# Kernel optimization log

Measured on AMD Instinct MI355X. Metric: run time of the kernel, lower is better.

## Reference

```python
import jax, jax.numpy as jnp
import numpy as np

L, D, H, EXP = 6, 512, 8, 4
DH = D // H
EPS = 1e-3  # keras LayerNormalization default epsilon


def _layer_norm(x, gamma, beta):
    mu = jnp.mean(x, axis=-1, keepdims=True)
    var = jnp.mean(jnp.square(x - mu), axis=-1, keepdims=True)
    return (x - mu) * jax.lax.rsqrt(var + EPS) * gamma + beta


def setup_inputs() -> dict:
    key = jax.random.key(0)
    ks = jax.random.split(key, 10)
    B, S = 8, 1024
    s_attn = 1.0 / np.sqrt(D)
    s_ffn1 = 1.0 / np.sqrt(D)
    s_ffn2 = 1.0 / np.sqrt(D * EXP)
    return {
        "x": jax.random.normal(ks[0], (B, S, D), dtype=jnp.float32),
        "Wq": jax.random.normal(ks[1], (L, D, D), dtype=jnp.float32) * s_attn,
        "Wk": jax.random.normal(ks[2], (L, D, D), dtype=jnp.float32) * s_attn,
        "Wv": jax.random.normal(ks[3], (L, D, D), dtype=jnp.float32) * s_attn,
        "Wo": jax.random.normal(ks[4], (L, D, D), dtype=jnp.float32) * s_attn,
        "W1": jax.random.normal(ks[5], (L, D, D * EXP), dtype=jnp.float32) * s_ffn1,
        "b1": jnp.zeros((L, D * EXP), dtype=jnp.float32),
        "W2": jax.random.normal(ks[6], (L, D * EXP, D), dtype=jnp.float32) * s_ffn2,
        "b2": jnp.zeros((L, D), dtype=jnp.float32),
        "g_attn": jnp.ones((L, D), dtype=jnp.float32),
        "be_attn": jnp.zeros((L, D), dtype=jnp.float32),
        "g_ffn": jnp.ones((L, D), dtype=jnp.float32),
        "be_ffn": jnp.zeros((L, D), dtype=jnp.float32),
    }


def _self_attention(y, wq, wk, wv, wo):
    B, S, _ = y.shape
    q = (y @ wq).reshape(B, S, H, DH)
    k = (y @ wk).reshape(B, S, H, DH)
    v = (y @ wv).reshape(B, S, H, DH)
    scores = jnp.einsum("bqhd,bkhd->bhqk", q, k) / np.sqrt(float(DH))
    attn = jax.nn.softmax(scores, axis=-1)
    z = jnp.einsum("bhqk,bkhd->bqhd", attn, v).reshape(B, S, D)
    return z @ wo


def reference(x, Wq, Wk, Wv, Wo, W1, b1, W2, b2, g_attn, be_attn, g_ffn, be_ffn):
    encoded = x
    for l in range(L):
        # pre-LN self-attention + residual (dropout=identity at inference)
        attended = _layer_norm(encoded, g_attn[l], be_attn[l])
        attended = _self_attention(attended, Wq[l], Wk[l], Wv[l], Wo[l])
        attended = encoded + attended
        # pre-LN FFN + residual
        h = _layer_norm(attended, g_ffn[l], be_ffn[l])
        h = jax.nn.relu(h @ W1[l] + b1[l]) @ W2[l] + b2[l]
        encoded = attended + h
    return encoded
```

## Files before the change

kernel.cpp:

```cpp
#include <hip/hip_runtime.h>


#define SEQ 1024
#define ROWS 8192
#define QKVW 1536

using bf16x8 = __attribute__((ext_vector_type(8))) short;
using f32x4  = __attribute__((ext_vector_type(4))) float;

__device__ __forceinline__ unsigned short f2bf(float f) {
  union { float f; unsigned u; } v; v.f = f;
  unsigned r = v.u + 0x7FFFu + ((v.u >> 16) & 1u);
  return (unsigned short)(r >> 16);
}

__device__ __forceinline__ float exp2_fast(float x) {
  float r;
  asm("v_exp_f32 %0, %1" : "=v"(r) : "v"(x));
  return r;
}

__device__ __forceinline__ unsigned cvtpk_bf16(float a, float b) {
  unsigned r;
  asm("v_cvt_pk_bf16_f32 %0, %1, %2" : "=v"(r) : "v"(a), "v"(b));
  return r;
}

__device__ __forceinline__ void gl16(const void* g, void* l) {
  typedef const unsigned int __attribute__((address_space(1)))* GP;
  typedef unsigned int __attribute__((address_space(3)))* LP;
  __builtin_amdgcn_global_load_lds((GP)g, (LP)l, 16, 0, 0);
}

__global__ __launch_bounds__(256) void transpose_cast_k(
    const float* __restrict__ W, unsigned short* __restrict__ Wt,
    int K, int N, int lstride, float scale)
{
  __shared__ float tile[32][33];
  const int l = blockIdx.z;
  const float* Wl = W + (size_t)l * K * N;
  unsigned short* Wtl = Wt + (size_t)l * lstride;
  const int k0 = blockIdx.y * 32, n0 = blockIdx.x * 32;
  const int tx = threadIdx.x & 31, ty = threadIdx.x >> 5;
  #pragma unroll
  for (int i = ty; i < 32; i += 8)
    tile[i][tx] = Wl[(size_t)(k0 + i) * N + n0 + tx];
  __syncthreads();
  #pragma unroll
  for (int i = ty; i < 32; i += 8)
    Wtl[(size_t)(n0 + i) * K + k0 + tx] = f2bf(tile[tx][i] * scale);
}

__global__ __launch_bounds__(256) void ln_k(
    const float* __restrict__ x, const float* __restrict__ g,
    const float* __restrict__ be, unsigned short* __restrict__ y, int rows)
{
  const int wid = (blockIdx.x << 2) | (threadIdx.x >> 6);
  const int lane = threadIdx.x & 63;
  if (wid >= rows) return;
  const float4* xr = reinterpret_cast<const float4*>(x + (size_t)wid * 512);
  float4 a = xr[lane];
  float4 b = xr[lane + 64];
  float s = a.x + a.y + a.z + a.w + b.x + b.y + b.z + b.w;
  #pragma unroll
  for (int m = 32; m >= 1; m >>= 1) s += __shfl_xor(s, m);
  const float mu = s * (1.0f / 512.0f);
  const float d0 = a.x - mu, d1 = a.y - mu, d2 = a.z - mu, d3 = a.w - mu;
  const float e0 = b.x - mu, e1 = b.y - mu, e2 = b.z - mu, e3 = b.w - mu;
  float q = d0*d0 + d1*d1 + d2*d2 + d3*d3 + e0*e0 + e1*e1 + e2*e2 + e3*e3;
  #pragma unroll
  for (int m = 32; m >= 1; m >>= 1) q += __shfl_xor(q, m);
  const float inv = rsqrtf(q * (1.0f / 512.0f) + 1e-3f);
  const float4* gr = reinterpret_cast<const float4*>(g);
  const float4* br = reinterpret_cast<const float4*>(be);
  const float4 g0 = gr[lane], g1 = gr[lane + 64];
  const float4 h0 = br[lane], h1 = br[lane + 64];
  ushort4 o0, o1;
  o0.x = f2bf(d0 * inv * g0.x + h0.x);
  o0.y = f2bf(d1 * inv * g0.y + h0.y);
  o0.z = f2bf(d2 * inv * g0.z + h0.z);
  o0.w = f2bf(d3 * inv * g0.w + h0.w);
  o1.x = f2bf(e0 * inv * g1.x + h1.x);
  o1.y = f2bf(e1 * inv * g1.y + h1.y);
  o1.z = f2bf(e2 * inv * g1.z + h1.z);
  o1.w = f2bf(e3 * inv * g1.w + h1.w);
  *reinterpret_cast<ushort4*>(y + (size_t)wid * 512 + lane * 4) = o0;
  *reinterpret_cast<ushort4*>(y + (size_t)wid * 512 + (lane + 64) * 4) = o1;
}

template<bool RELU, bool HASBIAS, bool HASRES, bool OUTBF>
__global__ __launch_bounds__(256) void gemm128_k(
    const unsigned short* __restrict__ A,
    const unsigned short* __restrict__ Wt,
    const float* __restrict__ bias,
    const float* __restrict__ res,
    void* __restrict__ outp, int M, int N, int K)
{
  __shared__ __align__(16) unsigned short As0[4096], Bs0[4096];
  __shared__ __align__(16) unsigned short As1[4096], Bs1[4096];
  const int t = threadIdx.x;
  const int nwg = gridDim.x * gridDim.y;
  const int bid = blockIdx.y * gridDim.x + blockIdx.x;
  const int nid = (bid & 7) * (nwg >> 3) + (bid >> 3);
  const int bx = nid % gridDim.x, by = nid / gridDim.x;
  const int m0 = by * 128, n0 = bx * 128;
  const int w = t >> 6, lane = t & 63, llo = lane & 15, lhi = lane >> 4;
  const int wr = w >> 1, wc = w & 1;

  const int sr = t >> 2, sg = (t & 3) ^ ((t >> 3) & 3);
  const unsigned short* pa = &A[(size_t)(m0 + sr) * K + sg * 8];
  const unsigned short* pb = &Wt[(size_t)(n0 + sr) * K + sg * 8];

#define GSTAGE128(AsX, BsX, koff) do { \
    gl16(pa + (koff), &AsX[t * 8]); \
    gl16(pa + (size_t)64 * K + (koff), &AsX[2048 + t * 8]); \
    gl16(pb + (koff), &BsX[t * 8]); \
    gl16(pb + (size_t)64 * K + (koff), &BsX[2048 + t * 8]); \
  } while (0)

  const int pgo = (lhi ^ ((llo >> 1) & 3)) * 8;

#define GCOMP128(AsX, BsX) do { \
    bf16x8 af[4], bfr[4]; \
    _Pragma("unroll") \
    for (int f = 0; f < 4; f++) { \
      af[f]  = *reinterpret_cast<const bf16x8*>(&AsX[(wr * 64 + f * 16 + llo) * 32 + pgo]); \
      bfr[f] = *reinterpret_cast<const bf16x8*>(&BsX[(wc * 64 + f * 16 + llo) * 32 + pgo]); \
    } \
    _Pragma("unroll") \
    for (int fi = 0; fi < 4; fi++) \
      _Pragma("unroll") \
      for (int fj = 0; fj < 4; fj++) \
        acc[fi][fj] = __builtin_amdgcn_mfma_f32_16x16x32_bf16(af[fi], bfr[fj], acc[fi][fj], 0, 0, 0); \
  } while (0)

  f32x4 acc[4][4] = {};
  GSTAGE128(As0, Bs0, 0);
  for (int k0 = 0; k0 < K; k0 += 64) {
    __syncthreads();
    GSTAGE128(As1, Bs1, k0 + 32);
    GCOMP128(As0, Bs0);
    __syncthreads();
    if (k0 + 64 < K) GSTAGE128(As0, Bs0, k0 + 64);
    GCOMP128(As1, Bs1);
  }
#undef GSTAGE128
#undef GCOMP128

  const int row0 = m0 + wr * 64, col0 = n0 + wc * 64;
  #pragma unroll
  for (int fi = 0; fi < 4; fi++)
    #pragma unroll
    for (int fj = 0; fj < 4; fj++)
      #pragma unroll
      for (int i = 0; i < 4; i++) {
        const int row = row0 + fi * 16 + lhi * 4 + i;
        const int col = col0 + fj * 16 + llo;
        float v = acc[fi][fj][i];
        if (HASBIAS) v += bias[col];
        if (HASRES)  v += res[(size_t)row * N + col];
        if (RELU)    v = fmaxf(v, 0.0f);
        if (OUTBF) ((unsigned short*)outp)[(size_t)row * N + col] = f2bf(v);
        else       ((float*)outp)[(size_t)row * N + col] = v;
      }
}

template<bool RELU, bool HASBIAS, bool HASRES, bool OUTBF>
__global__ __launch_bounds__(256) void gemm64_k(
    const unsigned short* __restrict__ A,
    const unsigned short* __restrict__ Wt,
    const float* __restrict__ bias,
    const float* __restrict__ res,
    void* __restrict__ outp, int M, int N, int K)
{
  __shared__ __align__(16) unsigned short As0[2048], Bs0[4096];
  __shared__ __align__(16) unsigned short As1[2048], Bs1[4096];
  const int t = threadIdx.x;
  const int nwg = gridDim.x * gridDim.y;
  const int bid = blockIdx.y * gridDim.x + blockIdx.x;
  const int nid = (bid & 7) * (nwg >> 3) + (bid >> 3);
  const int bx = nid % gridDim.x, by = nid / gridDim.x;
  const int m0 = by * 64, n0 = bx * 128;
  const int w = t >> 6, lane = t & 63, llo = lane & 15, lhi = lane >> 4;
  const int wr = w >> 1, wc = w & 1;

  const int sr = t >> 2, sg = (t & 3) ^ ((t >> 3) & 3);
  const unsigned short* pa = &A[(size_t)(m0 + sr) * K + sg * 8];
  const unsigned short* pb = &Wt[(size_t)(n0 + sr) * K + sg * 8];

#define GSTAGE64(AsX, BsX, koff) do { \
    gl16(pa + (koff), &AsX[t * 8]); \
    gl16(pb + (koff), &BsX[t * 8]); \
    gl16(pb + (size_t)64 * K + (koff), &BsX[2048 + t * 8]); \
  } while (0)

  const int pgo = (lhi ^ ((llo >> 1) & 3)) * 8;

#define GCOMP64(AsX, BsX) do { \
    bf16x8 af[2], bfr[4]; \
    _Pragma("unroll") \
    for (int f = 0; f < 2; f++) \
      af[f] = *reinterpret_cast<const bf16x8*>(&AsX[(wr * 32 + f * 16 + llo) * 32 + pgo]); \
    _Pragma("unroll") \
    for (int f = 0; f < 4; f++) \
      bfr[f] = *reinterpret_cast<const bf16x8*>(&BsX[(wc * 64 + f * 16 + llo) * 32 + pgo]); \
    _Pragma("unroll") \
    for (int fi = 0; fi < 2; fi++) \
      _Pragma("unroll") \
      for (int fj = 0; fj < 4; fj++) \
        acc[fi][fj] = __builtin_amdgcn_mfma_f32_16x16x32_bf16(af[fi], bfr[fj], acc[fi][fj], 0, 0, 0); \
  } while (0)

  f32x4 acc[2][4] = {};
  GSTAGE64(As0, Bs0, 0);
  for (int k0 = 0; k0 < K; k0 += 64) {
    __syncthreads();
    GSTAGE64(As1, Bs1, k0 + 32);
    GCOMP64(As0, Bs0);
    __syncthreads();
    if (k0 + 64 < K) GSTAGE64(As0, Bs0, k0 + 64);
    GCOMP64(As1, Bs1);
  }
#undef GSTAGE64
#undef GCOMP64

  const int row0 = m0 + wr * 32, col0 = n0 + wc * 64;
  #pragma unroll
  for (int fi = 0; fi < 2; fi++)
    #pragma unroll
    for (int fj = 0; fj < 4; fj++)
      #pragma unroll
      for (int i = 0; i < 4; i++) {
        const int row = row0 + fi * 16 + lhi * 4 + i;
        const int col = col0 + fj * 16 + llo;
        float v = acc[fi][fj][i];
        if (HASBIAS) v += bias[col];
        if (HASRES)  v += res[(size_t)row * N + col];
        if (RELU)    v = fmaxf(v, 0.0f);
        if (OUTBF) ((unsigned short*)outp)[(size_t)row * N + col] = f2bf(v);
        else       ((float*)outp)[(size_t)row * N + col] = v;
      }
}

__global__ __launch_bounds__(256) void vtrans_k(
    const unsigned short* __restrict__ QKV, unsigned short* __restrict__ VT)
{
  __shared__ unsigned short tile[64][66];
  const int kt = blockIdx.x, bh = blockIdx.y;
  const int bb = bh >> 3, h = bh & 7;
  const int t = threadIdx.x;
  const int r = t >> 2, c0 = (t & 3) * 16;
  const unsigned short* src = &QKV[((size_t)bb * SEQ + kt * 64 + r) * QKVW + 1024 + h * 64 + c0];
  *reinterpret_cast<uint4*>(&tile[r][c0])     = *reinterpret_cast<const uint4*>(src);
  *reinterpret_cast<uint4*>(&tile[r][c0 + 8]) = *reinterpret_cast<const uint4*>(src + 8);
  __syncthreads();
  const int dv = t >> 2, kv0 = (t & 3) * 16;
  unsigned short tmp[16];
  #pragma unroll
  for (int j = 0; j < 16; j++) tmp[j] = tile[kv0 + j][dv];
  ushort4 o0, o1, o2, o3;
  o0.x = tmp[0];  o0.y = tmp[1];  o0.z = tmp[2];  o0.w = tmp[3];
  o1.x = tmp[4];  o1.y = tmp[5];  o1.z = tmp[6];  o1.w = tmp[7];
  o2.x = tmp[8];  o2.y = tmp[9];  o2.z = tmp[10]; o2.w = tmp[11];
  o3.x = tmp[12]; o3.y = tmp[13]; o3.z = tmp[14]; o3.w = tmp[15];
  unsigned short* dst = &VT[((size_t)bh * 64 + dv) * SEQ + kt * 64 + kv0];
  *reinterpret_cast<ushort4*>(dst)      = o0;
  *reinterpret_cast<ushort4*>(dst + 4)  = o1;
  *reinterpret_cast<ushort4*>(dst + 8)  = o2;
  *reinterpret_cast<ushort4*>(dst + 12) = o3;
}

__global__ __launch_bounds__(256) void attn_k(
    const unsigned short* __restrict__ QKV,
    const unsigned short* __restrict__ VT,
    unsigned short* __restrict__ Zb)
{
  __shared__ __align__(16) unsigned short Ks0[4096], Vs0[4096];
  __shared__ __align__(16) unsigned short Ks1[4096], Vs1[4096];
  __shared__ __align__(16) unsigned short Ps[4096];

  const int t = threadIdx.x;
  const int qt = blockIdx.x, h = blockIdx.y, bb = blockIdx.z;
  const int w = t >> 6, lane = t & 63, llo = lane & 15, lhi = lane >> 4;
  const size_t rowb = (size_t)bb * SEQ;
  const int kcol = 512 + h * 64;
  const size_t vtb = (size_t)(bb * 8 + h) * 64 * SEQ;

  bf16x8 aq[2];
  #pragma unroll
  for (int ds = 0; ds < 2; ds++)
    aq[ds] = *reinterpret_cast<const bf16x8*>(
        &QKV[(rowb + qt * 64 + w * 16 + llo) * QKVW + h * 64 + ds * 32 + lhi * 8]);

  const int cA = t, cB = 256 + t;
  const int gA = cA >> 6, lA = cA & 63, gB = cB >> 6, lB = cB & 63;
  const unsigned short* kpA = &QKV[(rowb + (gA >> 1) * 16 + (lA & 15)) * QKVW + kcol + (gA & 1) * 32 + (lA >> 4) * 8];
  const unsigned short* kpB = &QKV[(rowb + (gB >> 1) * 16 + (lB & 15)) * QKVW + kcol + (gB & 1) * 32 + (lB >> 4) * 8];
  const unsigned short* vpA = &VT[vtb + (size_t)((gA >> 1) * 16 + (lA & 15)) * SEQ + (gA & 1) * 32 + (lA >> 4) * 8];
  const unsigned short* vpB = &VT[vtb + (size_t)((gB >> 1) * 16 + (lB & 15)) * SEQ + (gB & 1) * 32 + (lB >> 4) * 8];

#define ASTAGE(KsX, VsX, ktt) do { \
    gl16(kpA + (size_t)(ktt) * 64 * QKVW, &KsX[cA * 8]); \
    gl16(kpB + (size_t)(ktt) * 64 * QKVW, &KsX[cB * 8]); \
    gl16(vpA + (ktt) * 64, &VsX[cA * 8]); \
    gl16(vpB + (ktt) * 64, &VsX[cB * 8]); \
  } while (0)

  const int psbase = w * 1024 + llo * 64;
  const int lsw = llo & 7;

#define ACOMP(KsX, VsX) do { \
    f32x4 s_[4]; \
    _Pragma("unroll") \
    for (int fj = 0; fj < 4; fj++) \
      _Pragma("unroll") \
      for (int i = 0; i < 4; i++) s_[fj][i] = -16.0f; \
    _Pragma("unroll") \
    for (int ds = 0; ds < 2; ds++) \
      _Pragma("unroll") \
      for (int fj = 0; fj < 4; fj++) { \
        bf16x8 bk = *reinterpret_cast<const bf16x8*>(&KsX[((fj * 2 + ds) * 64 + lane) * 8]); \
        s_[fj] = __builtin_amdgcn_mfma_f32_16x16x32_bf16(bk, aq[ds], s_[fj], 0, 0, 0); \
      } \
    _Pragma("unroll") \
    for (int fj = 0; fj < 4; fj++) { \
      const float p0 = exp2_fast(s_[fj][0]); \
      const float p1 = exp2_fast(s_[fj][1]); \
      const float p2 = exp2_fast(s_[fj][2]); \
      const float p3 = exp2_fast(s_[fj][3]); \
      l_ += (p0 + p1) + (p2 + p3); \
      uint2 uv; uv.x = cvtpk_bf16(p0, p1); uv.y = cvtpk_bf16(p2, p3); \
      const int pg = ((fj << 1) | (lhi >> 1)) ^ lsw; \
      *reinterpret_cast<uint2*>(&Ps[psbase + pg * 8 + (lhi & 1) * 4]) = uv; \
    } \
    _Pragma("unroll") \
    for (int ks = 0; ks < 2; ks++) { \
      bf16x8 ap = *reinterpret_cast<const bf16x8*>(&Ps[psbase + ((((ks << 2) | lhi) ^ lsw) << 3)]); \
      _Pragma("unroll") \
      for (int fo = 0; fo < 4; fo++) { \
        bf16x8 bv = *reinterpret_cast<const bf16x8*>(&VsX[((fo * 2 + ks) * 64 + lane) * 8]); \
        o_[fo] = __builtin_amdgcn_mfma_f32_16x16x32_bf16(ap, bv, o_[fo], 0, 0, 0); \
      } \
    } \
  } while (0)

  float l_ = 0.0f;
  f32x4 o_[4] = {};

  ASTAGE(Ks0, Vs0, 0);
  for (int kt = 0; kt < 16; kt += 2) {
    __syncthreads();
    ASTAGE(Ks1, Vs1, kt + 1);
    ACOMP(Ks0, Vs0);
    __syncthreads();
    if (kt + 2 < 16) ASTAGE(Ks0, Vs0, kt + 2);
    ACOMP(Ks1, Vs1);
  }
#undef ASTAGE
#undef ACOMP

  l_ += __shfl_xor(l_, 16);
  l_ += __shfl_xor(l_, 32);
  const float linv = 1.0f / l_;

  #pragma unroll
  for (int i = 0; i < 4; i++) {
    const float li = __shfl(linv, lhi * 4 + i);
    #pragma unroll
    for (int fo = 0; fo < 4; fo++) {
      const float v = o_[fo][i] * li;
      Zb[(rowb + qt * 64 + w * 16 + lhi * 4 + i) * 512 + h * 64 + fo * 16 + llo] = f2bf(v);
    }
  }
}

extern "C" void kernel_launch(void* const* d_in, const int* in_sizes, int n_in,
                              void* d_out, int out_size, void* d_ws, size_t ws_size,
                              hipStream_t stream)
{
  const float* x   = (const float*)d_in[0];
  const float* Wq  = (const float*)d_in[1];
  const float* Wk  = (const float*)d_in[2];
  const float* Wv  = (const float*)d_in[3];
  const float* Wo  = (const float*)d_in[4];
  const float* W1  = (const float*)d_in[5];
  const float* b1  = (const float*)d_in[6];
  const float* W2  = (const float*)d_in[7];
  const float* b2  = (const float*)d_in[8];
  const float* ga  = (const float*)d_in[9];
  const float* ba  = (const float*)d_in[10];
  const float* gf  = (const float*)d_in[11];
  const float* bfn = (const float*)d_in[12];
  float* out = (float*)d_out;

  char* p = (char*)d_ws;
  auto alloc = [&](size_t bytes) { void* r = (void*)p; p += (bytes + 255) & ~(size_t)255; return r; };
  float* E0 = (float*)alloc((size_t)ROWS * 512 * 4);
  float* E1 = (float*)alloc((size_t)ROWS * 512 * 4);
  unsigned short* Ybf   = (unsigned short*)alloc((size_t)ROWS * 512 * 2);
  unsigned short* QKVbf = (unsigned short*)alloc((size_t)ROWS * QKVW * 2);
  unsigned short* H1bf  = (unsigned short*)alloc((size_t)ROWS * 2048 * 2);
  unsigned short* VT    = H1bf;
  unsigned short* WtQKV = (unsigned short*)alloc(6ull * QKVW * 512 * 2);
  unsigned short* WtO   = (unsigned short*)alloc(6ull * 512 * 512 * 2);
  unsigned short* Wt1   = (unsigned short*)alloc(6ull * 2048 * 512 * 2);
  unsigned short* Wt2   = (unsigned short*)alloc(6ull * 512 * 2048 * 2);
  unsigned short* Zbf   = Ybf;

  const float qscale = 0.125f * 1.44269504f;
  transpose_cast_k<<<dim3(16, 16, 6), 256, 0, stream>>>(Wq, WtQKV,          512, 512,  QKVW * 512, qscale);
  transpose_cast_k<<<dim3(16, 16, 6), 256, 0, stream>>>(Wk, WtQKV + 262144, 512, 512,  QKVW * 512, 1.0f);
  transpose_cast_k<<<dim3(16, 16, 6), 256, 0, stream>>>(Wv, WtQKV + 524288, 512, 512,  QKVW * 512, 1.0f);
  transpose_cast_k<<<dim3(16, 16, 6), 256, 0, stream>>>(Wo, WtO,            512, 512,  262144,     1.0f);
  transpose_cast_k<<<dim3(64, 16, 6), 256, 0, stream>>>(W1, Wt1,            512, 2048, 1048576,    1.0f);
  transpose_cast_k<<<dim3(16, 64, 6), 256, 0, stream>>>(W2, Wt2,            2048, 512, 1048576,    1.0f);

  for (int l = 0; l < 6; l++) {
    const float* enc = (l == 0) ? x : E0;
    ln_k<<<2048, 256, 0, stream>>>(enc, ga + l * 512, ba + l * 512, Ybf, ROWS);
    gemm128_k<false, false, false, true><<<dim3(12, 64), 256, 0, stream>>>(
        Ybf, WtQKV + (size_t)l * QKVW * 512, nullptr, nullptr, QKVbf, ROWS, QKVW, 512);
    vtrans_k<<<dim3(16, 64), 256, 0, stream>>>(QKVbf, VT);
    attn_k<<<dim3(16, 8, 8), 256, 0, stream>>>(QKVbf, VT, Zbf);
    gemm64_k<false, false, true, false><<<dim3(4, 128), 256, 0, stream>>>(
        Zbf, WtO + (size_t)l * 262144, nullptr, enc, E1, ROWS, 512, 512);
    ln_k<<<2048, 256, 0, stream>>>(E1, gf + l * 512, bfn + l * 512, Ybf, ROWS);
    gemm128_k<true, true, false, true><<<dim3(16, 64), 256, 0, stream>>>(
        Ybf, Wt1 + (size_t)l * 1048576, b1 + l * 2048, nullptr, H1bf, ROWS, 2048, 512);
    gemm64_k<false, true, true, false><<<dim3(4, 128), 256, 0, stream>>>(
        H1bf, Wt2 + (size_t)l * 1048576, b2 + l * 512, E1, (l == 5) ? out : E0,
        ROWS, 512, 2048);
  }
}
```

Before: 883.8 us.

## Double attention query tile to 128 rows per block, reusing K/V tiles

The attention kernel now handles 128 query rows per block, with each wave computing two 16-row MFMA tiles that share every K and V fragment loaded from LDS. This halves global K/V traffic per query row and the number of blocks, and the grid is reordered so the head index varies fastest. In exchange it uses more registers and doubles LDS for P, and it launches fewer blocks (512), which could lower occupancy and latency hiding.

```diff
diff --git a/kernel.cpp b/kernel.cpp
--- a/kernel.cpp
+++ b/kernel.cpp
@@ -277,20 +277,22 @@
 {
   __shared__ __align__(16) unsigned short Ks0[4096], Vs0[4096];
   __shared__ __align__(16) unsigned short Ks1[4096], Vs1[4096];
-  __shared__ __align__(16) unsigned short Ps[4096];
+  __shared__ __align__(16) unsigned short Ps[8192];
 
   const int t = threadIdx.x;
-  const int qt = blockIdx.x, h = blockIdx.y, bb = blockIdx.z;
+  const int h = blockIdx.x, qt = blockIdx.y, bb = blockIdx.z;
   const int w = t >> 6, lane = t & 63, llo = lane & 15, lhi = lane >> 4;
   const size_t rowb = (size_t)bb * SEQ;
   const int kcol = 512 + h * 64;
   const size_t vtb = (size_t)(bb * 8 + h) * 64 * SEQ;
 
-  bf16x8 aq[2];
-  #pragma unroll
-  for (int ds = 0; ds < 2; ds++)
-    aq[ds] = *reinterpret_cast<const bf16x8*>(
-        &QKV[(rowb + qt * 64 + w * 16 + llo) * QKVW + h * 64 + ds * 32 + lhi * 8]);
+  bf16x8 aq[2][2];
+  #pragma unroll
+  for (int mi = 0; mi < 2; mi++)
+    #pragma unroll
+    for (int ds = 0; ds < 2; ds++)
+      aq[mi][ds] = *reinterpret_cast<const bf16x8*>(
+          &QKV[(rowb + qt * 128 + w * 32 + mi * 16 + llo) * QKVW + h * 64 + ds * 32 + lhi * 8]);
 
   const int cA = t, cB = 256 + t;
   const int gA = cA >> 6, lA = cA & 63, gB = cB >> 6, lB = cB & 63;
@@ -306,46 +308,54 @@
     gl16(vpB + (ktt) * 64, &VsX[cB * 8]); \
   } while (0)
 
-  const int psbase = w * 1024 + llo * 64;
+  const int psw = w * 2048;
   const int lsw = llo & 7;
 
 #define ACOMP(KsX, VsX) do { \
-    f32x4 s_[4]; \
-    _Pragma("unroll") \
-    for (int fj = 0; fj < 4; fj++) \
-      _Pragma("unroll") \
-      for (int i = 0; i < 4; i++) s_[fj][i] = -16.0f; \
+    f32x4 s_[2][4]; \
+    _Pragma("unroll") \
+    for (int mi = 0; mi < 2; mi++) \
+      _Pragma("unroll") \
+      for (int fj = 0; fj < 4; fj++) \
+        _Pragma("unroll") \
+        for (int i = 0; i < 4; i++) s_[mi][fj][i] = -16.0f; \
     _Pragma("unroll") \
     for (int ds = 0; ds < 2; ds++) \
       _Pragma("unroll") \
       for (int fj = 0; fj < 4; fj++) { \
         bf16x8 bk = *reinterpret_cast<const bf16x8*>(&KsX[((fj * 2 + ds) * 64 + lane) * 8]); \
-        s_[fj] = __builtin_amdgcn_mfma_f32_16x16x32_bf16(bk, aq[ds], s_[fj], 0, 0, 0); \
+        s_[0][fj] = __builtin_amdgcn_mfma_f32_16x16x32_bf16(bk, aq[0][ds], s_[0][fj], 0, 0, 0); \
+        s_[1][fj] = __builtin_amdgcn_mfma_f32_16x16x32_bf16(bk, aq[1][ds], s_[1][fj], 0, 0, 0); \
       } \
     _Pragma("unroll") \
-    for (int fj = 0; fj < 4; fj++) { \
-      const float p0 = exp2_fast(s_[fj][0]); \
-      const float p1 = exp2_fast(s_[fj][1]); \
-      const float p2 = exp2_fast(s_[fj][2]); \
-      const float p3 = exp2_fast(s_[fj][3]); \
-      l_ += (p0 + p1) + (p2 + p3); \
-      uint2 uv; uv.x = cvtpk_bf16(p0, p1); uv.y = cvtpk_bf16(p2, p3); \
-      const int pg = ((fj << 1) | (lhi >> 1)) ^ lsw; \
-      *reinterpret_cast<uint2*>(&Ps[psbase + pg * 8 + (lhi & 1) * 4]) = uv; \
-    } \
+    for (int mi = 0; mi < 2; mi++) \
+      _Pragma("unroll") \
+      for (int fj = 0; fj < 4; fj++) { \
+        const float p0 = exp2_fast(s_[mi][fj][0]); \
+        const float p1 = exp2_fast(s_[mi][fj][1]); \
+        const float p2 = exp2_fast(s_[mi][fj][2]); \
+        const float p3 = exp2_fast(s_[mi][fj][3]); \
+        l_[mi] += (p0 + p1) + (p2 + p3); \
+        uint2 uv; uv.x = cvtpk_bf16(p0, p1); uv.y = cvtpk_bf16(p2, p3); \
+        const int pg = ((fj << 1) | (lhi >> 1)) ^ lsw; \
+        *reinterpret_cast<uint2*>(&Ps[psw + (mi * 16 + llo) * 64 + pg * 8 + (lhi & 1) * 4]) = uv; \
+      } \
     _Pragma("unroll") \
     for (int ks = 0; ks < 2; ks++) { \
-      bf16x8 ap = *reinterpret_cast<const bf16x8*>(&Ps[psbase + ((((ks << 2) | lhi) ^ lsw) << 3)]); \
+      const int prg = (((ks << 2) | lhi) ^ lsw) << 3; \
+      bf16x8 ap0 = *reinterpret_cast<const bf16x8*>(&Ps[psw + llo * 64 + prg]); \
+      bf16x8 ap1 = *reinterpret_cast<const bf16x8*>(&Ps[psw + (16 + llo) * 64 + prg]); \
       _Pragma("unroll") \
       for (int fo = 0; fo < 4; fo++) { \
         bf16x8 bv = *reinterpret_cast<const bf16x8*>(&VsX[((fo * 2 + ks) * 64 + lane) * 8]); \
-        o_[fo] = __builtin_amdgcn_mfma_f32_16x16x32_bf16(ap, bv, o_[fo], 0, 0, 0); \
+        o_[0][fo] = __builtin_amdgcn_mfma_f32_16x16x32_bf16(ap0, bv, o_[0][fo], 0, 0, 0); \
+        o_[1][fo] = __builtin_amdgcn_mfma_f32_16x16x32_bf16(ap1, bv, o_[1][fo], 0, 0, 0); \
       } \
     } \
   } while (0)
 
-  float l_ = 0.0f;
-  f32x4 o_[4] = {};
+  float l_[2] = {0.0f, 0.0f};
+  f32x4 o_[2][4] = {};
 
   ASTAGE(Ks0, Vs0, 0);
   for (int kt = 0; kt < 16; kt += 2) {
@@ -359,19 +369,24 @@
 #undef ASTAGE
 #undef ACOMP
 
-  l_ += __shfl_xor(l_, 16);
-  l_ += __shfl_xor(l_, 32);
-  const float linv = 1.0f / l_;
-
-  #pragma unroll
-  for (int i = 0; i < 4; i++) {
-    const float li = __shfl(linv, lhi * 4 + i);
+  #pragma unroll
+  for (int mi = 0; mi < 2; mi++) {
+    l_[mi] += __shfl_xor(l_[mi], 16);
+    l_[mi] += __shfl_xor(l_[mi], 32);
+    l_[mi] = 1.0f / l_[mi];
+  }
+
+  #pragma unroll
+  for (int mi = 0; mi < 2; mi++)
     #pragma unroll
-    for (int fo = 0; fo < 4; fo++) {
-      const float v = o_[fo][i] * li;
-      Zb[(rowb + qt * 64 + w * 16 + lhi * 4 + i) * 512 + h * 64 + fo * 16 + llo] = f2bf(v);
+    for (int i = 0; i < 4; i++) {
+      const float li = __shfl(l_[mi], lhi * 4 + i);
+      #pragma unroll
+      for (int fo = 0; fo < 4; fo++) {
+        const float v = o_[mi][fo][i] * li;
+        Zb[(rowb + qt * 128 + w * 32 + mi * 16 + lhi * 4 + i) * 512 + h * 64 + fo * 16 + llo] = f2bf(v);
+      }
     }
-  }
 }
 
 extern "C" void kernel_launch(void* const* d_in, const int* in_sizes, int n_in,
@@ -421,7 +436,7 @@
     gemm128_k<false, false, false, true><<<dim3(12, 64), 256, 0, stream>>>(
         Ybf, WtQKV + (size_t)l * QKVW * 512, nullptr, nullptr, QKVbf, ROWS, QKVW, 512);
     vtrans_k<<<dim3(16, 64), 256, 0, stream>>>(QKVbf, VT);
-    attn_k<<<dim3(16, 8, 8), 256, 0, stream>>>(QKVbf, VT, Zbf);
+    attn_k<<<dim3(8, 8, 8), 256, 0, stream>>>(QKVbf, VT, Zbf);
     gemm64_k<false, false, true, false><<<dim3(4, 128), 256, 0, stream>>>(
         Zbf, WtO + (size_t)l * 262144, nullptr, enc, E1, ROWS, 512, 512);
     ln_k<<<2048, 256, 0, stream>>>(E1, gf + l * 512, bfn + l * 512, Ybf, ROWS);
```

Result: faster. 818.4 us (-7.4%).
